# Kernel optimization log

Hardware: AMD Instinct MI355X
Metric: run time of the kernel (lower is better)

## Reference

```python
import jax, jax.numpy as jnp
import numpy as np

N_NODES = 100000
N_EDGES = 1600000
D_IN = 128
D_OUT = 128


def setup_inputs() -> dict:
    key = jax.random.key(0)
    ks = jax.random.split(key, 7)
    x = jax.random.normal(ks[0], (N_NODES, D_IN), dtype=jnp.float32)
    y = jax.random.normal(ks[1], (N_NODES, D_OUT), dtype=jnp.float32)
    edge_src = jax.random.randint(ks[2], (N_EDGES,), 0, N_NODES, dtype=jnp.int32)
    edge_dst = jax.random.randint(ks[3], (N_EDGES,), 0, N_NODES, dtype=jnp.int32)
    adj_vals = jax.random.uniform(ks[4], (N_EDGES,), dtype=jnp.float32)
    weight = jax.random.normal(ks[5], (D_IN, D_OUT), dtype=jnp.float32) * (1.0 / np.sqrt(D_IN))
    bias = jax.random.normal(ks[6], (D_OUT,), dtype=jnp.float32) * 0.01
    return {"x": x, "y": y, "edge_src": edge_src, "edge_dst": edge_dst,
            "adj_vals": adj_vals, "weight": weight, "bias": bias}


def reference(x, y, edge_src, edge_dst, adj_vals, weight, bias):
    # GraphConvolution: support = x @ W ; out = spmm(adj, support) + bias
    support = x @ weight                      # [N, d_out]
    msgs = support[edge_src] * adj_vals[:, None]   # [E, d_out] gather + scale
    agg = jax.ops.segment_sum(msgs, edge_dst, num_segments=N_NODES)  # [N, d_out]
    gc_out = agg + bias
    # ResGCN epilogue: relu(gc_out + y); dropout is identity in eval (p=0.0)
    return jax.nn.relu(gc_out + y)
```

## Files before the change

kernel.cpp:

```cpp
#include <hip/hip_runtime.h>

#define D 128
#define CE 8192
#define NB_MAX 1024
#define MAXC 512
#define EBUF 3072
#define CHUNK 1024
#define WTP 136


typedef __attribute__((ext_vector_type(8))) short bf16x8;
typedef __attribute__((ext_vector_type(4))) float f32x4;

__device__ __forceinline__ unsigned short f2bf(float f) {
  unsigned u = __float_as_uint(f);
  unsigned r = (u + 0x7fffu + ((u >> 16) & 1u)) >> 16;
  return (unsigned short)r;
}

__device__ __forceinline__ int wave_iscan(int v) {
  const int lane = threadIdx.x & 63;
#pragma unroll
  for (int off = 1; off < 64; off <<= 1) {
    int u = __shfl_up(v, off, 64);
    if (lane >= off) v += u;
  }
  return v;
}

__device__ __forceinline__ int seg_find(const int* pref, int nC, int i) {
  int lo = 0, hi = nC;
  while (hi - lo > 1) {
    int mid = (lo + hi) >> 1;
    if (pref[mid] <= i) lo = mid; else hi = mid;
  }
  return lo;
}

__global__ __launch_bounds__(256) void convert_kernel(
    const float4* __restrict__ x4, ushort4* __restrict__ xb4, int n4, int nxblk,
    const float* __restrict__ w, unsigned short* __restrict__ wt) {
  int bid = blockIdx.x;
  if (bid < nxblk) {
    int i = bid * 256 + threadIdx.x;
    if (i < n4) {
      float4 v = x4[i];
      ushort4 r;
      r.x = f2bf(v.x);
      r.y = f2bf(v.y);
      r.z = f2bf(v.z);
      r.w = f2bf(v.w);
      xb4[i] = r;
    }
  } else {
    int idx = (bid - nxblk) * 256 + threadIdx.x;
    int n = idx >> 7, k = idx & 127;
    wt[n * WTP + k] = f2bf(w[k * D + n]);
  }
}

__global__ __launch_bounds__(1024) void chunk_sort_kernel(
    const int* __restrict__ src, const int* __restrict__ dst,
    const float* __restrict__ adj, int2* __restrict__ edges,
    unsigned short* __restrict__ ofs, int nE, int nB) {
  __shared__ int2 stage[CE];
  __shared__ int h[NB_MAX + 4];
  __shared__ int wsum[16];
  const int t = threadIdx.x;
  const int c = blockIdx.x;
  const int e0 = c * CE;
  const int n = min(CE, nE - e0);
  const int lane = t & 63, wid = t >> 6;

  for (int i = t; i < NB_MAX + 4; i += 1024) h[i] = 0;
  __syncthreads();

  int dreg[8];
#pragma unroll
  for (int k = 0; k < 8; ++k) {
    int i = k * 1024 + t;
    if (i < n) {
      int d = dst[e0 + i];
      dreg[k] = d;
      atomicAdd(&h[d >> 7], 1);
    }
  }
  __syncthreads();

  int v = h[t];
  int inc = wave_iscan(v);
  if (lane == 63) wsum[wid] = inc;
  __syncthreads();
  if (wid == 0) {
    int p = (lane < 16) ? wsum[lane] : 0;
    int pi = wave_iscan(p);
    if (lane < 16) wsum[lane] = pi;
  }
  __syncthreads();
  h[t] = inc - v + (wid ? wsum[wid - 1] : 0);
  __syncthreads();

  unsigned short* o = ofs + (size_t)c * (nB + 1);
  for (int i = t; i <= nB; i += 1024)
    o[i] = (unsigned short)(i < NB_MAX ? h[i] : n);
  __syncthreads();

#pragma unroll
  for (int k = 0; k < 8; ++k) {
    int i = k * 1024 + t;
    if (i < n) {
      int d = dreg[k];
      int pos = atomicAdd(&h[d >> 7], 1);
      int2 ev;
      ev.x = src[e0 + i] | ((d & 127) << 17);
      ev.y = __float_as_int(adj[e0 + i]);
      stage[pos] = ev;
    }
  }
  __syncthreads();

  for (int i = t; i < n; i += 1024) edges[e0 + i] = stage[i];
}

__global__ __launch_bounds__(256) void bucket_gather_kernel(
    const int2* __restrict__ tmp, const unsigned short* __restrict__ ofs,
    const uint2* __restrict__ xb, char* out, int nC, int nB, int nNodes) {
  __shared__ int2 ebuf[EBUF];
  __shared__ int segst[MAXC];
  __shared__ int pref[MAXC + 1];
  __shared__ int cnt[128];
  __shared__ int cur[128];
  __shared__ int sstart[128];
  __shared__ int w4[4];
  const int t = threadIdx.x;
  const int b = blockIdx.x;
  const int lane = t & 63, wid = t >> 6;

  const int c0 = 2 * t, c1 = 2 * t + 1;
  int n0 = 0, n1 = 0;
  if (c0 < nC) {
    int s0 = ofs[(size_t)c0 * (nB + 1) + b];
    int s1 = ofs[(size_t)c0 * (nB + 1) + b + 1];
    segst[c0] = c0 * CE + s0;
    n0 = s1 - s0;
  }
  if (c1 < nC) {
    int s0 = ofs[(size_t)c1 * (nB + 1) + b];
    int s1 = ofs[(size_t)c1 * (nB + 1) + b + 1];
    segst[c1] = c1 * CE + s0;
    n1 = s1 - s0;
  }
  int tt = n0 + n1;
  int inc = wave_iscan(tt);
  if (lane == 63) w4[wid] = inc;
  __syncthreads();
  int add = 0;
  for (int i = 0; i < wid; ++i) add += w4[i];
  int incl = inc + add;
  int excl = incl - tt;
  if (c0 < nC) pref[c0] = excl;
  if (c1 < nC) pref[c1] = excl + n0;
  if (t == 255) pref[nC] = incl;
  __syncthreads();
  const int m = pref[nC];

  const int gi = t >> 5;
  const int q = t & 31;
  float4 acc[16];
#pragma unroll
  for (int k = 0; k < 16; ++k) acc[k] = make_float4(0.f, 0.f, 0.f, 0.f);

  for (int w0 = 0; w0 < m; w0 += EBUF) {
    const int w1 = min(m, w0 + EBUF);
    if (t < 128) cnt[t] = 0;
    __syncthreads();

    for (int i = w0 + t; i < w1; i += 256) {
      int lo = seg_find(pref, nC, i);
      int sx = ((const int*)tmp)[(size_t)(segst[lo] + (i - pref[lo])) * 2];
      atomicAdd(&cnt[(sx >> 17) & 127], 1);
    }
    __syncthreads();

    int cv = (t < 128) ? cnt[t] : 0;
    int cinc = wave_iscan(cv);
    if (t == 63) w4[0] = cinc;
    __syncthreads();
    int cst = cinc - cv + ((t >= 64 && t < 128) ? w4[0] : 0);
    if (t < 128) {
      sstart[t] = cst;
      cur[t] = cst;
    }
    __syncthreads();

    for (int i = w0 + t; i < w1; i += 256) {
      int lo = seg_find(pref, nC, i);
      int2 ev = tmp[segst[lo] + (i - pref[lo])];
      int pos = atomicAdd(&cur[(ev.x >> 17) & 127], 1);
      ebuf[pos] = ev;
    }
    __syncthreads();

#pragma unroll
    for (int k = 0; k < 16; ++k) {
      const int dl = gi * 16 + k;
      int j = sstart[dl];
      const int e = cur[dl];
      for (; j + 3 < e; j += 4) {
        int2 e0 = ebuf[j], e1 = ebuf[j + 1], e2 = ebuf[j + 2], e3 = ebuf[j + 3];
        float a0 = __int_as_float(e0.y), a1 = __int_as_float(e1.y);
        float a2 = __int_as_float(e2.y), a3 = __int_as_float(e3.y);
        uint2 v0 = xb[(size_t)(e0.x & 0x1FFFF) * 32 + q];
        uint2 v1 = xb[(size_t)(e1.x & 0x1FFFF) * 32 + q];
        uint2 v2 = xb[(size_t)(e2.x & 0x1FFFF) * 32 + q];
        uint2 v3 = xb[(size_t)(e3.x & 0x1FFFF) * 32 + q];
        acc[k].x = fmaf(a0, __uint_as_float(v0.x << 16), acc[k].x);
        acc[k].y = fmaf(a0, __uint_as_float(v0.x & 0xffff0000u), acc[k].y);
        acc[k].z = fmaf(a0, __uint_as_float(v0.y << 16), acc[k].z);
        acc[k].w = fmaf(a0, __uint_as_float(v0.y & 0xffff0000u), acc[k].w);
        acc[k].x = fmaf(a1, __uint_as_float(v1.x << 16), acc[k].x);
        acc[k].y = fmaf(a1, __uint_as_float(v1.x & 0xffff0000u), acc[k].y);
        acc[k].z = fmaf(a1, __uint_as_float(v1.y << 16), acc[k].z);
        acc[k].w = fmaf(a1, __uint_as_float(v1.y & 0xffff0000u), acc[k].w);
        acc[k].x = fmaf(a2, __uint_as_float(v2.x << 16), acc[k].x);
        acc[k].y = fmaf(a2, __uint_as_float(v2.x & 0xffff0000u), acc[k].y);
        acc[k].z = fmaf(a2, __uint_as_float(v2.y << 16), acc[k].z);
        acc[k].w = fmaf(a2, __uint_as_float(v2.y & 0xffff0000u), acc[k].w);
        acc[k].x = fmaf(a3, __uint_as_float(v3.x << 16), acc[k].x);
        acc[k].y = fmaf(a3, __uint_as_float(v3.x & 0xffff0000u), acc[k].y);
        acc[k].z = fmaf(a3, __uint_as_float(v3.y << 16), acc[k].z);
        acc[k].w = fmaf(a3, __uint_as_float(v3.y & 0xffff0000u), acc[k].w);
      }
      for (; j < e; ++j) {
        int2 e0 = ebuf[j];
        float a0 = __int_as_float(e0.y);
        uint2 v0 = xb[(size_t)(e0.x & 0x1FFFF) * 32 + q];
        acc[k].x = fmaf(a0, __uint_as_float(v0.x << 16), acc[k].x);
        acc[k].y = fmaf(a0, __uint_as_float(v0.x & 0xffff0000u), acc[k].y);
        acc[k].z = fmaf(a0, __uint_as_float(v0.y << 16), acc[k].z);
        acc[k].w = fmaf(a0, __uint_as_float(v0.y & 0xffff0000u), acc[k].w);
      }
    }
    __syncthreads();
  }

#pragma unroll
  for (int k = 0; k < 16; ++k) {
    int g = b * 128 + gi * 16 + k;
    if (g < nNodes) {
      uint2 pk;
      pk.x = (unsigned)f2bf(acc[k].x) | ((unsigned)f2bf(acc[k].y) << 16);
      pk.y = (unsigned)f2bf(acc[k].z) | ((unsigned)f2bf(acc[k].w) << 16);
      ((uint2*)(out + (size_t)g * 512))[q] = pk;
    }
  }
}

__global__ __launch_bounds__(256) void gemm_mfma_kernel(
    const char* aggb, const unsigned short* __restrict__ wt,
    const float* __restrict__ y, const float* __restrict__ bias,
    float* out, int nNodes) {
  __shared__ unsigned short sWt[D * WTP];
  const int t = threadIdx.x;
  for (int i = t; i < D * WTP / 8; i += 256)
    ((int4*)sWt)[i] = ((const int4*)wt)[i];
  __syncthreads();

  const int w = t >> 6, l = t & 63;
  const int quad = l >> 4, m = l & 15;
  const int row0 = blockIdx.x * 128 + w * 32;

  const int ar0 = min(row0 + m, nNodes - 1);
  const int ar1 = min(row0 + 16 + m, nNodes - 1);
  const char* pa0 = aggb + (size_t)ar0 * 512;
  const char* pa1 = aggb + (size_t)ar1 * 512;

  f32x4 acc0[8], acc1[8];
#pragma unroll
  for (int nt = 0; nt < 8; ++nt) {
    acc0[nt] = (f32x4){0.f, 0.f, 0.f, 0.f};
    acc1[nt] = (f32x4){0.f, 0.f, 0.f, 0.f};
  }

#pragma unroll
  for (int ks = 0; ks < 4; ++ks) {
    const int kof = ks * 32 + quad * 8;
    bf16x8 a0 = *(const bf16x8*)(pa0 + kof * 2);
    bf16x8 a1 = *(const bf16x8*)(pa1 + kof * 2);
#pragma unroll
    for (int nt = 0; nt < 8; ++nt) {
      bf16x8 b = *(const bf16x8*)&sWt[(nt * 16 + m) * WTP + kof];
      acc0[nt] = __builtin_amdgcn_mfma_f32_16x16x32_bf16(a0, b, acc0[nt], 0, 0, 0);
      acc1[nt] = __builtin_amdgcn_mfma_f32_16x16x32_bf16(a1, b, acc1[nt], 0, 0, 0);
    }
  }

  float bv[8];
#pragma unroll
  for (int nt = 0; nt < 8; ++nt) bv[nt] = bias[nt * 16 + m];

#pragma unroll
  for (int s = 0; s < 2; ++s) {
#pragma unroll
    for (int r = 0; r < 4; ++r) {
      int row = row0 + s * 16 + quad * 4 + r;
      if (row >= nNodes) continue;
      const float* yr = y + (size_t)row * D;
      float* orow = out + (size_t)row * D;
#pragma unroll
      for (int nt = 0; nt < 8; ++nt) {
        int c = nt * 16 + m;
        float v = (s == 0 ? acc0[nt][r] : acc1[nt][r]) + yr[c] + bv[nt];
        orow[c] = fmaxf(v, 0.f);
      }
    }
  }
}

__global__ __launch_bounds__(256) void zero_counts_kernel(int* __restrict__ c, int n) {
  int i = blockIdx.x * 256 + threadIdx.x;
  if (i < n) c[i] = 0;
}

__global__ __launch_bounds__(256) void hist_kernel(
    const int* __restrict__ dst, int* __restrict__ counts, int nE) {
  int e = blockIdx.x * 256 + threadIdx.x;
  if (e < nE) atomicAdd(&counts[dst[e]], 1);
}

__global__ __launch_bounds__(256) void scan_partial_kernel(
    const int* __restrict__ counts, int* __restrict__ chunk_sum, int n) {
  __shared__ int sdata[256];
  int b = blockIdx.x, t = threadIdx.x;
  int base = b * CHUNK + t * 4;
  int s = 0;
#pragma unroll
  for (int k = 0; k < 4; ++k) {
    int i = base + k;
    if (i < n) s += counts[i];
  }
  sdata[t] = s;
  __syncthreads();
  for (int off = 128; off > 0; off >>= 1) {
    if (t < off) sdata[t] += sdata[t + off];
    __syncthreads();
  }
  if (t == 0) chunk_sum[b] = sdata[0];
}

__global__ void scan_chunks_kernel(const int* __restrict__ chunk_sum,
                                   int* __restrict__ chunk_off,
                                   int* __restrict__ row_start, int nchunks, int n) {
  if (threadIdx.x == 0 && blockIdx.x == 0) {
    int run = 0;
    for (int i = 0; i < nchunks; ++i) {
      chunk_off[i] = run;
      run += chunk_sum[i];
    }
    row_start[n] = run;
  }
}

__global__ __launch_bounds__(256) void scan_final_kernel(
    const int* __restrict__ counts, const int* __restrict__ chunk_off,
    int* __restrict__ row_start, int* __restrict__ cursor, int n) {
  __shared__ int sdata[256];
  int b = blockIdx.x, t = threadIdx.x;
  int base = b * CHUNK + t * 4;
  int c[4] = {0, 0, 0, 0};
#pragma unroll
  for (int k = 0; k < 4; ++k) {
    int i = base + k;
    if (i < n) c[k] = counts[i];
  }
  int tsum = c[0] + c[1] + c[2] + c[3];
  sdata[t] = tsum;
  __syncthreads();
  for (int off = 1; off < 256; off <<= 1) {
    int v = (t >= off) ? sdata[t - off] : 0;
    __syncthreads();
    sdata[t] += v;
    __syncthreads();
  }
  int run = sdata[t] - tsum + chunk_off[b];
#pragma unroll
  for (int k = 0; k < 4; ++k) {
    int i = base + k;
    if (i < n) {
      row_start[i] = run;
      cursor[i] = run;
      run += c[k];
    }
  }
}

__global__ __launch_bounds__(256) void scatter_sort_kernel(
    const int* __restrict__ src, const int* __restrict__ dst,
    const float* __restrict__ adj, int* __restrict__ cursor,
    int2* __restrict__ edges, int nE) {
  int e = blockIdx.x * 256 + threadIdx.x;
  if (e >= nE) return;
  int d = dst[e];
  int2 ev;
  ev.x = src[e];
  ev.y = __float_as_int(adj[e]);
  int pos = atomicAdd(&cursor[d], 1);
  edges[pos] = ev;
}

__global__ __launch_bounds__(256) void gather_fp32_kernel(
    const float* __restrict__ x, const int* __restrict__ row_start,
    const int2* __restrict__ edges, float* __restrict__ out, int nNodes) {
  int g = (blockIdx.x * 256 + threadIdx.x) >> 5;
  int q = threadIdx.x & 31;
  if (g >= nNodes) return;
  int beg = row_start[g], end = row_start[g + 1];
  const float4* x4 = (const float4*)x;
  float4 acc = make_float4(0.f, 0.f, 0.f, 0.f);
  for (int j = beg; j < end; ++j) {
    int2 e0 = edges[j];
    float a0 = __int_as_float(e0.y);
    float4 v0 = x4[(size_t)e0.x * 32 + q];
    acc.x = fmaf(a0, v0.x, acc.x);
    acc.y = fmaf(a0, v0.y, acc.y);
    acc.z = fmaf(a0, v0.z, acc.z);
    acc.w = fmaf(a0, v0.w, acc.w);
  }
  ((float4*)out)[(size_t)g * 32 + q] = acc;
}

__global__ __launch_bounds__(256) void zero_kernel(float4* __restrict__ out, int n4) {
  int i = blockIdx.x * 256 + threadIdx.x;
  if (i < n4) out[i] = make_float4(0.f, 0.f, 0.f, 0.f);
}

__global__ __launch_bounds__(256) void scatter_atomic_kernel(
    const float* __restrict__ x, const int* __restrict__ src,
    const int* __restrict__ dst, const float* __restrict__ adj,
    float* __restrict__ out, int nE) {
  int tid = blockIdx.x * 256 + threadIdx.x;
  int e = tid >> 5;
  int q = tid & 31;
  if (e >= nE) return;
  int s = src[e];
  int d = dst[e];
  float a = adj[e];
  float4 v = ((const float4*)x)[(size_t)s * 32 + q];
  float* o = out + (size_t)d * D + q * 4;
  atomicAdd(o + 0, v.x * a);
  atomicAdd(o + 1, v.y * a);
  atomicAdd(o + 2, v.z * a);
  atomicAdd(o + 3, v.w * a);
}

__global__ __launch_bounds__(256) void gemm_fused_kernel(
    float* __restrict__ out, const float* __restrict__ w,
    const float* __restrict__ y, const float* __restrict__ bias, int nrows) {
  __shared__ float sW[D * D];
  __shared__ float sA[32 * D];
  const int tid = threadIdx.x;
  const int row0 = blockIdx.x * 32;

  const float4* w4 = (const float4*)w;
  float4* sW4 = (float4*)sW;
  for (int i = tid; i < D * D / 4; i += 256) sW4[i] = w4[i];

  const int nrow_blk = min(32, nrows - row0);
  const float4* out4_base = (const float4*)(out + (size_t)row0 * D);
  float4* sA4 = (float4*)sA;
  for (int i = tid; i < nrow_blk * 32; i += 256) sA4[i] = out4_base[i];
  __syncthreads();

  const int cg = tid & 31;
  const int rs = tid >> 5;

  float4 acc[4];
#pragma unroll
  for (int r = 0; r < 4; ++r) acc[r] = make_float4(0.f, 0.f, 0.f, 0.f);

#pragma unroll 4
  for (int k4 = 0; k4 < 32; ++k4) {
    float4 wv0 = sW4[(k4 * 4 + 0) * 32 + cg];
    float4 wv1 = sW4[(k4 * 4 + 1) * 32 + cg];
    float4 wv2 = sW4[(k4 * 4 + 2) * 32 + cg];
    float4 wv3 = sW4[(k4 * 4 + 3) * 32 + cg];
#pragma unroll
    for (int r = 0; r < 4; ++r) {
      float4 xv = sA4[(rs + r * 8) * 32 + k4];
      acc[r].x = fmaf(xv.x, wv0.x, acc[r].x);
      acc[r].y = fmaf(xv.x, wv0.y, acc[r].y);
      acc[r].z = fmaf(xv.x, wv0.z, acc[r].z);
      acc[r].w = fmaf(xv.x, wv0.w, acc[r].w);
      acc[r].x = fmaf(xv.y, wv1.x, acc[r].x);
      acc[r].y = fmaf(xv.y, wv1.y, acc[r].y);
      acc[r].z = fmaf(xv.y, wv1.z, acc[r].z);
      acc[r].w = fmaf(xv.y, wv1.w, acc[r].w);
      acc[r].x = fmaf(xv.z, wv2.x, acc[r].x);
      acc[r].y = fmaf(xv.z, wv2.y, acc[r].y);
      acc[r].z = fmaf(xv.z, wv2.z, acc[r].z);
      acc[r].w = fmaf(xv.z, wv2.w, acc[r].w);
      acc[r].x = fmaf(xv.w, wv3.x, acc[r].x);
      acc[r].y = fmaf(xv.w, wv3.y, acc[r].y);
      acc[r].z = fmaf(xv.w, wv3.z, acc[r].z);
      acc[r].w = fmaf(xv.w, wv3.w, acc[r].w);
    }
  }

  const float4* y4 = (const float4*)y;
  const float4* b4 = (const float4*)bias;
  float4* o4 = (float4*)out;
  float4 bv = b4[cg];
#pragma unroll
  for (int r = 0; r < 4; ++r) {
    int row = row0 + rs + r * 8;
    if (row < nrows) {
      float4 yv = y4[(size_t)row * 32 + cg];
      float4 res;
      res.x = fmaxf(acc[r].x + yv.x + bv.x, 0.f);
      res.y = fmaxf(acc[r].y + yv.y + bv.y, 0.f);
      res.z = fmaxf(acc[r].z + yv.z + bv.z, 0.f);
      res.w = fmaxf(acc[r].w + yv.w + bv.w, 0.f);
      o4[(size_t)row * 32 + cg] = res;
    }
  }
}

extern "C" void kernel_launch(void* const* d_in, const int* in_sizes, int n_in,
                              void* d_out, int out_size, void* d_ws, size_t ws_size,
                              hipStream_t stream) {
  const float* x    = (const float*)d_in[0];
  const float* y    = (const float*)d_in[1];
  const int*   esrc = (const int*)d_in[2];
  const int*   edst = (const int*)d_in[3];
  const float* adj  = (const float*)d_in[4];
  const float* w    = (const float*)d_in[5];
  const float* bias = (const float*)d_in[6];
  float* out = (float*)d_out;

  const int nNodes = in_sizes[0] / D;
  const int nE = in_sizes[2];
  const int n4 = nNodes * (D / 4);
  const int nB = (nNodes + 127) >> 7;
  const int nC = (nE + CE - 1) / CE;

  const size_t ofs_bytes = (((size_t)nC * (nB + 1) * 2) + 15) & ~(size_t)15;
  const size_t wt_bytes  = (size_t)D * WTP * 2;
  const size_t tmp_bytes = (size_t)nC * CE * 8;
  const size_t xb_bytes  = (size_t)nNodes * D * 2;
  const size_t need1 = ofs_bytes + wt_bytes + tmp_bytes + xb_bytes;

  const int nchunks = (nNodes + CHUNK - 1) / CHUNK;
  const size_t e2_bytes  = (size_t)nE * 8;
  const size_t int_bytes = (size_t)(3 * nNodes + 1 + 2 * nchunks) * 4;
  const size_t need2 = e2_bytes + int_bytes;

  if (ws_size >= need1 && nNodes <= NB_MAX * 128 && nC <= MAXC) {
    char* p = (char*)d_ws;
    unsigned short* ofs = (unsigned short*)p;   p += ofs_bytes;
    unsigned short* wt = (unsigned short*)p;    p += wt_bytes;
    int2* tmp = (int2*)p;                       p += tmp_bytes;
    ushort4* xb4 = (ushort4*)p;

    const int nxblk = (n4 + 255) / 256;
    chunk_sort_kernel<<<nC, 1024, 0, stream>>>(esrc, edst, adj, tmp, ofs, nE, nB);
    convert_kernel<<<nxblk + 64, 256, 0, stream>>>((const float4*)x, xb4, n4,
                                                   nxblk, w, wt);
    bucket_gather_kernel<<<nB, 256, 0, stream>>>(
        tmp, ofs, (const uint2*)xb4, (char*)d_out, nC, nB, nNodes);
    gemm_mfma_kernel<<<(nNodes + 127) / 128, 256, 0, stream>>>(
        (const char*)d_out, wt, y, bias, out, nNodes);
  } else if (ws_size >= need2) {
    char* base = (char*)d_ws;
    int2* edges = (int2*)base;
    int* counts = (int*)(base + e2_bytes);
    int* row_start = counts + nNodes;
    int* cursor = row_start + nNodes + 1;
    int* chunk_sum = cursor + nNodes;
    int* chunk_off = chunk_sum + nchunks;

    zero_counts_kernel<<<(nNodes + 255) / 256, 256, 0, stream>>>(counts, nNodes);
    hist_kernel<<<(nE + 255) / 256, 256, 0, stream>>>(edst, counts, nE);
    scan_partial_kernel<<<nchunks, 256, 0, stream>>>(counts, chunk_sum, nNodes);
    scan_chunks_kernel<<<1, 64, 0, stream>>>(chunk_sum, chunk_off, row_start,
                                             nchunks, nNodes);
    scan_final_kernel<<<nchunks, 256, 0, stream>>>(counts, chunk_off, row_start,
                                                   cursor, nNodes);
    scatter_sort_kernel<<<(nE + 255) / 256, 256, 0, stream>>>(
        esrc, edst, adj, cursor, edges, nE);
    gather_fp32_kernel<<<(nNodes * 32 + 255) / 256, 256, 0, stream>>>(
        x, row_start, edges, out, nNodes);
    gemm_fused_kernel<<<(nNodes + 31) / 32, 256, 0, stream>>>(out, w, y, bias,
                                                              nNodes);
  } else {
    zero_kernel<<<(n4 + 255) / 256, 256, 0, stream>>>((float4*)out, n4);
    scatter_atomic_kernel<<<((size_t)nE * 32 + 255) / 256, 256, 0, stream>>>(
        x, esrc, edst, adj, out, nE);
    gemm_fused_kernel<<<(nNodes + 31) / 32, 256, 0, stream>>>(out, w, y, bias,
                                                              nNodes);
  }
}
```

Before: 305.1 us.

## Fuse x/W bf16 conversion into chunk sort kernel and reuse histogram ranks

Result: faster. 296.1 us (-3.0%).

```diff
diff --git a/kernel.cpp b/kernel.cpp
--- a/kernel.cpp
+++ b/kernel.cpp
@@ -37,37 +37,42 @@
   return lo;
 }
 
-__global__ __launch_bounds__(256) void convert_kernel(
-    const float4* __restrict__ x4, ushort4* __restrict__ xb4, int n4, int nxblk,
-    const float* __restrict__ w, unsigned short* __restrict__ wt) {
-  int bid = blockIdx.x;
-  if (bid < nxblk) {
-    int i = bid * 256 + threadIdx.x;
-    if (i < n4) {
-      float4 v = x4[i];
-      ushort4 r;
-      r.x = f2bf(v.x);
-      r.y = f2bf(v.y);
-      r.z = f2bf(v.z);
-      r.w = f2bf(v.w);
-      xb4[i] = r;
-    }
-  } else {
-    int idx = (bid - nxblk) * 256 + threadIdx.x;
-    int n = idx >> 7, k = idx & 127;
-    wt[n * WTP + k] = f2bf(w[k * D + n]);
-  }
-}
-
-__global__ __launch_bounds__(1024) void chunk_sort_kernel(
+__global__ __launch_bounds__(1024) void sort_convert_kernel(
     const int* __restrict__ src, const int* __restrict__ dst,
     const float* __restrict__ adj, int2* __restrict__ edges,
-    unsigned short* __restrict__ ofs, int nE, int nB) {
+    unsigned short* __restrict__ ofs, int nE, int nB, int nC,
+    const float4* __restrict__ x4, ushort4* __restrict__ xb4, int n4,
+    int nxblk, const float* __restrict__ w, unsigned short* __restrict__ wt) {
   __shared__ int2 stage[CE];
   __shared__ int h[NB_MAX + 4];
   __shared__ int wsum[16];
+  const int bid = blockIdx.x;
   const int t = threadIdx.x;
-  const int c = blockIdx.x;
+
+  if (bid >= nC) {
+    int b2 = bid - nC;
+    if (b2 < nxblk) {
+      int i = b2 * 1024 + t;
+      if (i < n4) {
+        float4 v = x4[i];
+        ushort4 r;
+        r.x = f2bf(v.x);
+        r.y = f2bf(v.y);
+        r.z = f2bf(v.z);
+        r.w = f2bf(v.w);
+        xb4[i] = r;
+      }
+    } else {
+      int idx = (b2 - nxblk) * 1024 + t;
+      if (idx < D * D) {
+        int n = idx >> 7, k = idx & 127;
+        wt[n * WTP + k] = f2bf(w[k * D + n]);
+      }
+    }
+    return;
+  }
+
+  const int c = bid;
   const int e0 = c * CE;
   const int n = min(CE, nE - e0);
   const int lane = t & 63, wid = t >> 6;
@@ -81,8 +86,8 @@
     int i = k * 1024 + t;
     if (i < n) {
       int d = dst[e0 + i];
-      dreg[k] = d;
-      atomicAdd(&h[d >> 7], 1);
+      int rank = atomicAdd(&h[d >> 7], 1);
+      dreg[k] = d | (rank << 17);
     }
   }
   __syncthreads();
@@ -103,14 +108,15 @@
   unsigned short* o = ofs + (size_t)c * (nB + 1);
   for (int i = t; i <= nB; i += 1024)
     o[i] = (unsigned short)(i < NB_MAX ? h[i] : n);
-  __syncthreads();
 
 #pragma unroll
   for (int k = 0; k < 8; ++k) {
     int i = k * 1024 + t;
     if (i < n) {
-      int d = dreg[k];
-      int pos = atomicAdd(&h[d >> 7], 1);
+      int dr = dreg[k];
+      int d = dr & 0x1FFFF;
+      int rank = ((unsigned)dr) >> 17;
+      int pos = h[d >> 7] + rank;
       int2 ev;
       ev.x = src[e0 + i] | ((d & 127) << 17);
       ev.y = __float_as_int(adj[e0 + i]);
@@ -561,10 +567,11 @@
     int2* tmp = (int2*)p;                       p += tmp_bytes;
     ushort4* xb4 = (ushort4*)p;
 
-    const int nxblk = (n4 + 255) / 256;
-    chunk_sort_kernel<<<nC, 1024, 0, stream>>>(esrc, edst, adj, tmp, ofs, nE, nB);
-    convert_kernel<<<nxblk + 64, 256, 0, stream>>>((const float4*)x, xb4, n4,
-                                                   nxblk, w, wt);
+    const int nxblk = (n4 + 1023) / 1024;
+    const int wtblk = (D * D + 1023) / 1024;
+    sort_convert_kernel<<<nC + nxblk + wtblk, 1024, 0, stream>>>(
+        esrc, edst, adj, tmp, ofs, nE, nB, nC,
+        (const float4*)x, xb4, n4, nxblk, w, wt);
     bucket_gather_kernel<<<nB, 256, 0, stream>>>(
         tmp, ofs, (const uint2*)xb4, (char*)d_out, nC, nB, nNodes);
     gemm_mfma_kernel<<<(nNodes + 127) / 128, 256, 0, stream>>>(
```
